# Performance work log

Hardware: AMD Instinct MI355X
Metric: run time of the kernel (lower is better)

Reference implementation:

```python
import jax, jax.numpy as jnp
import numpy as np


def setup_inputs() -> dict:
    key = jax.random.key(0)
    ks = jax.random.split(key, 9)
    B, Lq, Lk, D = 8, 2048, 2048, 768
    s = 1.0 / np.sqrt(D)
    return {
        "queries": jax.random.normal(ks[0], (B, Lq, D), dtype=jnp.float32),
        "values": jax.random.normal(ks[1], (B, Lk, D), dtype=jnp.float32),
        "mask": jax.random.randint(ks[2], (B, Lq, Lk), 0, 2) > 0,
        "Wq": jax.random.normal(ks[3], (D, D), dtype=jnp.float32) * s,
        "bq": jax.random.normal(ks[4], (D,), dtype=jnp.float32) * s,
        "Wk": jax.random.normal(ks[5], (D, D), dtype=jnp.float32) * s,
        "bk": jax.random.normal(ks[6], (D,), dtype=jnp.float32) * s,
        "Wv": jax.random.normal(ks[7], (D, D), dtype=jnp.float32) * s,
        "bv": jax.random.normal(ks[8], (D,), dtype=jnp.float32) * s,
    }


def reference(queries, values, mask, Wq, bq, Wk, bk, Wv, bv):
    NEG = jnp.asarray(-1e9, queries.dtype)
    # torch Linear: x @ W.T + b
    q = jnp.einsum("bld,ed->ble", queries, Wq) + bq
    v = jnp.einsum("bld,ed->ble", values, Wv) + bv
    # NOTE (faithful to source): keys are the key-projection of the
    # already value-projected tensor.
    k = jnp.einsum("bld,ed->ble", v, Wk) + bk
    score = jnp.einsum("bqd,bkd->bqk", q, k)  # [B, Lq, Lk]
    score = jnp.where(mask, score, NEG)
    attn = jax.nn.sigmoid(score)  # sigmoid attention, no normalization
    context = jnp.einsum("bqk,bkd->bqd", attn, v)
    return context
```

## Files before the change

### kernel.cpp

```cpp
#include <hip/hip_runtime.h>
#include <hip/hip_bf16.h>

typedef __bf16 bf16_t;
typedef __bf16 bf16x8 __attribute__((ext_vector_type(8)));
typedef __bf16 bf16x4 __attribute__((ext_vector_type(4)));
typedef float  f32x4  __attribute__((ext_vector_type(4)));

#define LDS_DST(p) ((__attribute__((address_space(3))) void*)(p))
#define GLB_SRC(p) ((const __attribute__((address_space(1))) void*)(p))

#define SBAR()   asm volatile("s_barrier" ::: "memory")
#define WVM8()   asm volatile("s_waitcnt vmcnt(8)" ::: "memory")
#define WVM4()   asm volatile("s_waitcnt vmcnt(4)" ::: "memory")
#define WVM0()   asm volatile("s_waitcnt vmcnt(0)" ::: "memory")
#define SP1()    __builtin_amdgcn_s_setprio(1)
#define SP0()    __builtin_amdgcn_s_setprio(0)

__global__ void __launch_bounds__(256)
convert_kernel(const float* __restrict__ q_in, const float* __restrict__ v_in,
               const float* __restrict__ wq_in, const float* __restrict__ wk_in,
               const float* __restrict__ wv_in,
               bf16_t* __restrict__ qb, bf16_t* __restrict__ vb,
               bf16_t* __restrict__ wqb, bf16_t* __restrict__ wkb,
               bf16_t* __restrict__ wvb) {
  const int tid = threadIdx.x;
  int r = blockIdx.x;
  const float* in; bf16_t* out; int base;
  if (r < 6144) {
    in = (r < 3072) ? q_in : v_in;
    out = (r < 3072) ? qb : vb;
    base = (r % 3072) * 1024;
  } else {
    r -= 6144;
    in = (r < 144) ? wq_in : (r < 288 ? wk_in : wv_in);
    out = (r < 144) ? wqb : (r < 288 ? wkb : wvb);
    base = (r % 144) * 1024;
  }
#pragma unroll
  for (int j = 0; j < 4; ++j) {
    const int i = base + j * 256 + tid;
    const float4 v = reinterpret_cast<const float4*>(in)[i];
    bf16x4 o;
    o[0] = (bf16_t)v.x; o[1] = (bf16_t)v.y; o[2] = (bf16_t)v.z; o[3] = (bf16_t)v.w;
    reinterpret_cast<bf16x4*>(out)[i] = o;
  }
}

__global__ void __launch_bounds__(256)
transpose_bf16_kernel(const bf16_t* __restrict__ in, bf16_t* __restrict__ out,
                      int R, int C) {
  __shared__ bf16_t tile[64][72];
  const long base = (long)blockIdx.z * R * C;
  const bf16_t* ib = in + base;
  bf16_t* ob = out + base;
  const int r0 = blockIdx.x * 64, c0 = blockIdx.y * 64;
  const int tid = threadIdx.x;
  const int rr = tid >> 3, cg = tid & 7;
#pragma unroll
  for (int p = 0; p < 2; ++p) {
    int row = p * 32 + rr;
    bf16x8 v = *reinterpret_cast<const bf16x8*>(ib + (long)(r0 + row) * C + c0 + cg * 8);
    *reinterpret_cast<bf16x8*>(&tile[row][cg * 8]) = v;
  }
  __syncthreads();
#pragma unroll
  for (int p = 0; p < 2; ++p) {
    int c = p * 32 + rr;
    bf16x8 v;
#pragma unroll
    for (int i = 0; i < 8; ++i) v[i] = tile[cg * 8 + i][c];
    *reinterpret_cast<bf16x8*>(ob + (long)(c0 + c) * R + r0 + cg * 8) = v;
  }
}


__device__ __forceinline__ void read_A(const char* smem, int off, bf16x8 (&af)[8], int xk0) {
#pragma unroll
  for (int mf = 0; mf < 4; ++mf)
#pragma unroll
    for (int kk = 0; kk < 2; ++kk)
      af[mf * 2 + kk] = *reinterpret_cast<const bf16x8*>(
          smem + off + mf * 2048 + (kk ? (xk0 ^ 64) : xk0));
}

__device__ __forceinline__ void read_B(const char* smem, int off, bf16x8 (&bf_)[4], int xk0) {
#pragma unroll
  for (int nf = 0; nf < 2; ++nf)
#pragma unroll
    for (int kk = 0; kk < 2; ++kk)
      bf_[nf * 2 + kk] = *reinterpret_cast<const bf16x8*>(
          smem + off + nf * 2048 + (kk ? (xk0 ^ 64) : xk0));
}

template <int MH, int NH>
__device__ __forceinline__ void mfma_q(const bf16x8 (&af)[8], const bf16x8 (&bf_)[4],
                                       f32x4 (&acc)[8][4]) {
#pragma unroll
  for (int mf = 0; mf < 4; ++mf)
#pragma unroll
    for (int nf = 0; nf < 2; ++nf)
#pragma unroll
      for (int kk = 0; kk < 2; ++kk)
        acc[MH * 4 + mf][NH * 2 + nf] = __builtin_amdgcn_mfma_f32_16x16x32_bf16(
            af[mf * 2 + kk], bf_[nf * 2 + kk], acc[MH * 4 + mf][NH * 2 + nf], 0, 0, 0);
}

#define STAGE_A(slot, mh, kt) do {                                            \
  _Pragma("unroll") for (int j_ = 0; j_ < 2; ++j_)                            \
    __builtin_amdgcn_global_load_lds(                                         \
        GLB_SRC(pA + (long)(j_ * 128 + (mh) * 64) * K + (kt)),                \
        LDS_DST(smem + (slot) * 65536 + (arow0 + j_ * 128 + (mh) * 64) * 128),\
        16, 0, 0);                                                            \
} while (0)

#define STAGE_B(slot, nh, kt) do {                                            \
  _Pragma("unroll") for (int j_ = 0; j_ < 2; ++j_)                            \
    __builtin_amdgcn_global_load_lds(                                         \
        GLB_SRC(pB + (long)(j_ * 128 + (nh) * 32) * K + (kt)),                \
        LDS_DST(smem + (slot) * 65536 + 32768 +                               \
                (brow0 + j_ * 128 + (nh) * 32) * 128),                        \
        16, 0, 0);                                                            \
} while (0)

#define EWRITE(RD, eb) do {                                                   \
  _Pragma("unroll") for (int fi = 0; fi < 2; ++fi)                            \
  _Pragma("unroll") for (int nf = 0; nf < 4; ++nf)                            \
  _Pragma("unroll") for (int r = 0; r < 4; ++r) {                             \
    const int lr2 = wr * 32 + fi * 16 + lg * 4 + r;                           \
    (eb)[lr2 * 256 + wc * 64 + nf * 16 + l15] = acc[(RD) * 2 + fi][nf][r];    \
  }                                                                           \
} while (0)

template <int MODE>
__global__ void __launch_bounds__(512, 2)
gemm8p_kernel(const bf16_t* __restrict__ A, const bf16_t* __restrict__ B,
              const float* __restrict__ bias, const int* __restrict__ mask,
              void* __restrict__ Cout, int M, int N, int K,
              long sA, long sB, long sC, long sMask,
              const bf16_t* __restrict__ A2, const bf16_t* __restrict__ B2,
              const float* __restrict__ bias2, void* __restrict__ C2) {
  __shared__ __align__(1024) char smem[131072];

  const int gx = gridDim.x, gy = gridDim.y;
  int f0 = blockIdx.x + gx * (blockIdx.y + gy * blockIdx.z);
  const int nwg = gx * gy * (int)gridDim.z;
  const int q8 = nwg >> 3, r8 = nwg & 7;
  const int xcd = f0 & 7, idx = f0 >> 3;
  int f1 = (xcd < r8 ? xcd * (q8 + 1) : r8 * (q8 + 1) + (xcd - r8) * q8) + idx;
  int bxi, byi, bz;
  if constexpr (MODE == 1) {
    bxi = f1 & 7;
    const int byL = (f1 >> 3) & 1;
    const int st = (f1 >> 4) & 3;
    bz = f1 >> 6;
    byi = st * 2 + byL;
  } else {
    byi = f1 % gy;
    const int t = f1 / gy;
    bxi = t % gx;
    bz = t / gx;
  }

  const bf16_t* Ab; const bf16_t* Bb;
  const float* biasp = bias; void* Cp = Cout;
  if constexpr (MODE == 0) {
    if (bz) { Ab = A2; Bb = B2; biasp = bias2; Cp = C2; }
    else    { Ab = A;  Bb = B; }
  } else {
    Ab = A + bz * sA; Bb = B + bz * sB;
  }
  const int bm = bxi * 256, bn = byi * 256;
  const int tid = threadIdx.x;
  const int wave = tid >> 6, lane = tid & 63;
  const int wr = wave >> 2, wc = wave & 3;
  const int l15 = lane & 15, lg = lane >> 4;
  const int xk0 = (lg * 16) ^ ((lane & 7) << 4);
  const int NT = K >> 6;

  const int lr = lane >> 3;
  const int cgs = ((lane & 7) ^ lr) * 8;
  const int arow0 = wave * 8;
  const int brow0 = (wave >> 2) * 64 + (wave & 3) * 8;
  const bf16_t* pA = Ab + (long)(bm + arow0 + lr) * K + cgs;
  const bf16_t* pB = Bb + (long)(bn + brow0 + lr) * K + cgs;

  const int aoff = wr * 16384 + l15 * 128;
  const int boff = 32768 + wc * 8192 + l15 * 128;

  f32x4 acc[8][4] = {};
  bf16x8 afX[8], bfB[4], bf0[4];

  STAGE_A(0, 0, 0); STAGE_B(0, 0, 0); STAGE_B(0, 1, 0); STAGE_A(0, 1, 0);
  STAGE_A(1, 0, 64); STAGE_B(1, 0, 64);
  STAGE_B(1, 1, 64); STAGE_A(1, 1, 64);
  WVM8();
  SBAR();
  read_A(smem, aoff + 0, afX, xk0);
  read_B(smem, boff + 0, bf0, xk0);

  int slot = 0;
  for (int t = 0; t + 2 < NT; ++t) {
    const int so = slot * 65536, sn = (slot ^ 1) * 65536;
    const int k2 = (t + 2) << 6;
    read_B(smem, so + boff + 4096, bfB, xk0);
    STAGE_A(slot, 0, k2); STAGE_B(slot, 0, k2);
    SP1(); mfma_q<0, 0>(afX, bf0, acc); SP0();
    SP1(); mfma_q<0, 1>(afX, bfB, acc); SP0();
    read_A(smem, so + aoff + 8192, afX, xk0);
    WVM8(); SBAR();
    SP1(); mfma_q<1, 1>(afX, bfB, acc); SP0();
    SP1(); mfma_q<1, 0>(afX, bf0, acc); SP0();
    read_A(smem, sn + aoff + 0, afX, xk0);
    read_B(smem, sn + boff + 0, bf0, xk0);
    STAGE_B(slot, 1, k2); STAGE_A(slot, 1, k2);
    WVM8(); SBAR();
    slot ^= 1;
  }

  {
    const int so = slot * 65536, sn = (slot ^ 1) * 65536;
    read_B(smem, so + boff + 4096, bfB, xk0);
    SP1(); mfma_q<0, 0>(afX, bf0, acc); SP0();
    SP1(); mfma_q<0, 1>(afX, bfB, acc); SP0();
    read_A(smem, so + aoff + 8192, afX, xk0);
    WVM4(); SBAR();
    SP1(); mfma_q<1, 1>(afX, bfB, acc); SP0();
    SP1(); mfma_q<1, 0>(afX, bf0, acc); SP0();
    read_A(smem, sn + aoff + 0, afX, xk0);
    read_B(smem, sn + boff + 0, bf0, xk0);
    WVM0(); SBAR();
    read_B(smem, sn + boff + 4096, bfB, xk0);
    SP1(); mfma_q<0, 0>(afX, bf0, acc); SP0();
    SP1(); mfma_q<0, 1>(afX, bfB, acc); SP0();
    read_A(smem, sn + aoff + 8192, afX, xk0);
    SP1(); mfma_q<1, 1>(afX, bfB, acc); SP0();
    SP1(); mfma_q<1, 0>(afX, bf0, acc); SP0();
  }

  float* eb0 = (float*)smem;
  float* eb1 = (float*)(smem + 65536);
  const int lrow = tid >> 3, t7 = tid & 7;
  const int growt0 = lrow + ((lrow >> 5) * 96);
  int4 m4a[8], m4b[8];
  if constexpr (MODE == 1) {
    const int* mrow = mask + bz * sMask + (long)(bm + growt0) * N + bn;
#pragma unroll
    for (int q = 0; q < 8; ++q)
      m4a[q] = *reinterpret_cast<const int4*>(mrow + (q * 8 + t7) * 4);
  }
  EWRITE(0, eb0);
  __syncthreads();
#pragma unroll
  for (int rd = 0; rd < 4; ++rd) {
    if constexpr (MODE == 1) {
      if (rd < 3) {
        const int* mrow =
            mask + bz * sMask + (long)(bm + (rd + 1) * 32 + growt0) * N + bn;
        if ((rd & 1) == 0) {
#pragma unroll
          for (int q = 0; q < 8; ++q)
            m4b[q] = *reinterpret_cast<const int4*>(mrow + (q * 8 + t7) * 4);
        } else {
#pragma unroll
          for (int q = 0; q < 8; ++q)
            m4a[q] = *reinterpret_cast<const int4*>(mrow + (q * 8 + t7) * 4);
        }
      }
    }
    if (rd < 3) {
      if ((rd & 1) == 0) { EWRITE(rd + 1, eb1); } else { EWRITE(rd + 1, eb0); }
    }
    const float* eb = ((rd & 1) == 0) ? eb0 : eb1;
    const long rowbase = (long)(bm + rd * 32 + growt0) * N + bn;
#pragma unroll
    for (int q = 0; q < 8; ++q) {
      const int c4 = (q * 8 + t7) * 4;
      const f32x4 v = *reinterpret_cast<const f32x4*>(&eb[lrow * 256 + c4]);
      if constexpr (MODE == 1) {
        const int4 mq = ((rd & 1) == 0) ? m4a[q] : m4b[q];
        bf16x4 o;
        o[0] = (bf16_t)(mq.x ? __builtin_amdgcn_rcpf(1.f + __expf(-v[0])) : 0.f);
        o[1] = (bf16_t)(mq.y ? __builtin_amdgcn_rcpf(1.f + __expf(-v[1])) : 0.f);
        o[2] = (bf16_t)(mq.z ? __builtin_amdgcn_rcpf(1.f + __expf(-v[2])) : 0.f);
        o[3] = (bf16_t)(mq.w ? __builtin_amdgcn_rcpf(1.f + __expf(-v[3])) : 0.f);
        *reinterpret_cast<bf16x4*>((bf16_t*)Cp + bz * sC + rowbase + c4) = o;
      } else if constexpr (MODE == 0) {
        const f32x4 b4 = *reinterpret_cast<const f32x4*>(biasp + bn + c4);
        bf16x4 o;
        o[0] = (bf16_t)(v[0] + b4[0]); o[1] = (bf16_t)(v[1] + b4[1]);
        o[2] = (bf16_t)(v[2] + b4[2]); o[3] = (bf16_t)(v[3] + b4[3]);
        *reinterpret_cast<bf16x4*>((bf16_t*)Cp + bz * sC + rowbase + c4) = o;
      } else {
        *reinterpret_cast<f32x4*>((float*)Cp + bz * sC + rowbase + c4) = v;
      }
    }
    __syncthreads();
  }
}

extern "C" void kernel_launch(void* const* d_in, const int* in_sizes, int n_in,
                              void* d_out, int out_size, void* d_ws, size_t ws_size,
                              hipStream_t stream) {
  const float* queries = (const float*)d_in[0];
  const float* values  = (const float*)d_in[1];
  const int*   mask    = (const int*)d_in[2];
  const float* Wq = (const float*)d_in[3];
  const float* bq = (const float*)d_in[4];
  const float* Wk = (const float*)d_in[5];
  const float* bk = (const float*)d_in[6];
  const float* Wv = (const float*)d_in[7];
  const float* bv = (const float*)d_in[8];

  char* ws = (char*)d_ws;
  bf16_t* qb  = (bf16_t*)(ws + 0);
  bf16_t* vb  = (bf16_t*)(ws + 25165824);
  bf16_t* wqb = (bf16_t*)(ws + 50331648);
  bf16_t* wkb = (bf16_t*)(ws + 51511296);
  bf16_t* wvb = (bf16_t*)(ws + 52690944);
  bf16_t* qp  = (bf16_t*)(ws + 53870592);
  bf16_t* vp  = (bf16_t*)(ws + 79036416);
  bf16_t* kp  = (bf16_t*)(ws + 104202240);
  bf16_t* vpT = (bf16_t*)(ws + 129368064);
  bf16_t* P   = (bf16_t*)(ws + 154533888);

  convert_kernel<<<6576, 256, 0, stream>>>(queries, values, Wq, Wk, Wv,
                                           qb, vb, wqb, wkb, wvb);

  const dim3 blk2(512);

  gemm8p_kernel<0><<<dim3(64, 3, 2), blk2, 0, stream>>>(
      qb, wqb, bq, nullptr, qp, 16384, 768, 768, 0, 0, 0, 0,
      vb, wvb, bv, vp);
  gemm8p_kernel<0><<<dim3(64, 3, 1), blk2, 0, stream>>>(
      vp, wkb, bk, nullptr, kp, 16384, 768, 768, 0, 0, 0, 0,
      vp, wkb, bk, kp);

  transpose_bf16_kernel<<<dim3(32, 12, 8), 256, 0, stream>>>(vp, vpT, 2048, 768);

  gemm8p_kernel<1><<<dim3(8, 8, 8), blk2, 0, stream>>>(
      qp, kp, nullptr, mask, P, 2048, 2048, 768,
      (long)2048 * 768, (long)2048 * 768, (long)2048 * 2048, (long)2048 * 2048,
      nullptr, nullptr, nullptr, nullptr);

  gemm8p_kernel<2><<<dim3(8, 3, 8), blk2, 0, stream>>>(
      P, vpT, nullptr, nullptr, d_out, 2048, 768, 2048,
      (long)2048 * 2048, (long)768 * 2048, (long)2048 * 768, 0,
      nullptr, nullptr, nullptr, nullptr);
}
```

Baseline: 253.5 us.

## Fuse V transpose into the V-projection GEMM epilogue and swizzle epilogue LDS

Removes the standalone bf16 transpose kernel. The V-projection GEMM epilogue now also writes a transposed copy of its output (with bias) straight to vpT, reading it back from the staged LDS tile. The MODE 0 epilogue staging buffer gains an XOR swizzle so that the column-wise reads avoid bank conflicts. This saves one launch and a full read and write of vp, but adds strided 16-byte global stores and extra LDS reads to the projection epilogue.

```diff
diff --git a/kernel.cpp b/kernel.cpp
--- a/kernel.cpp
+++ b/kernel.cpp
@@ -46,33 +46,6 @@
   }
 }
 
-__global__ void __launch_bounds__(256)
-transpose_bf16_kernel(const bf16_t* __restrict__ in, bf16_t* __restrict__ out,
-                      int R, int C) {
-  __shared__ bf16_t tile[64][72];
-  const long base = (long)blockIdx.z * R * C;
-  const bf16_t* ib = in + base;
-  bf16_t* ob = out + base;
-  const int r0 = blockIdx.x * 64, c0 = blockIdx.y * 64;
-  const int tid = threadIdx.x;
-  const int rr = tid >> 3, cg = tid & 7;
-#pragma unroll
-  for (int p = 0; p < 2; ++p) {
-    int row = p * 32 + rr;
-    bf16x8 v = *reinterpret_cast<const bf16x8*>(ib + (long)(r0 + row) * C + c0 + cg * 8);
-    *reinterpret_cast<bf16x8*>(&tile[row][cg * 8]) = v;
-  }
-  __syncthreads();
-#pragma unroll
-  for (int p = 0; p < 2; ++p) {
-    int c = p * 32 + rr;
-    bf16x8 v;
-#pragma unroll
-    for (int i = 0; i < 8; ++i) v[i] = tile[cg * 8 + i][c];
-    *reinterpret_cast<bf16x8*>(ob + (long)(c0 + c) * R + r0 + cg * 8) = v;
-  }
-}
-
 
 __device__ __forceinline__ void read_A(const char* smem, int off, bf16x8 (&af)[8], int xk0) {
 #pragma unroll
@@ -131,6 +104,16 @@
   }                                                                           \
 } while (0)
 
+#define EWRITE_S(RD, eb) do {                                                 \
+  _Pragma("unroll") for (int fi = 0; fi < 2; ++fi)                            \
+  _Pragma("unroll") for (int nf = 0; nf < 4; ++nf)                            \
+  _Pragma("unroll") for (int r = 0; r < 4; ++r) {                             \
+    const int lr2 = wr * 32 + fi * 16 + lg * 4 + r;                           \
+    const int cS = (wc * 64 + nf * 16 + l15) ^ ((lr2 & 7) << 2);              \
+    (eb)[lr2 * 256 + cS] = acc[(RD) * 2 + fi][nf][r];                         \
+  }                                                                           \
+} while (0)
+
 template <int MODE>
 __global__ void __launch_bounds__(512, 2)
 gemm8p_kernel(const bf16_t* __restrict__ A, const bf16_t* __restrict__ B,
@@ -138,7 +121,8 @@
               void* __restrict__ Cout, int M, int N, int K,
               long sA, long sB, long sC, long sMask,
               const bf16_t* __restrict__ A2, const bf16_t* __restrict__ B2,
-              const float* __restrict__ bias2, void* __restrict__ C2) {
+              const float* __restrict__ bias2, void* __restrict__ C2,
+              bf16_t* __restrict__ Ct) {
   __shared__ __align__(1024) char smem[131072];
 
   const int gx = gridDim.x, gy = gridDim.y;
@@ -241,6 +225,7 @@
   float* eb1 = (float*)(smem + 65536);
   const int lrow = tid >> 3, t7 = tid & 7;
   const int growt0 = lrow + ((lrow >> 5) * 96);
+  const bool doT = (MODE == 0) && (bz != 0) && (Ct != nullptr);
   int4 m4a[8], m4b[8];
   if constexpr (MODE == 1) {
     const int* mrow = mask + bz * sMask + (long)(bm + growt0) * N + bn;
@@ -248,7 +233,7 @@
     for (int q = 0; q < 8; ++q)
       m4a[q] = *reinterpret_cast<const int4*>(mrow + (q * 8 + t7) * 4);
   }
-  EWRITE(0, eb0);
+  if constexpr (MODE == 0) { EWRITE_S(0, eb0); } else { EWRITE(0, eb0); }
   __syncthreads();
 #pragma unroll
   for (int rd = 0; rd < 4; ++rd) {
@@ -268,14 +253,19 @@
       }
     }
     if (rd < 3) {
-      if ((rd & 1) == 0) { EWRITE(rd + 1, eb1); } else { EWRITE(rd + 1, eb0); }
+      if constexpr (MODE == 0) {
+        if ((rd & 1) == 0) { EWRITE_S(rd + 1, eb1); } else { EWRITE_S(rd + 1, eb0); }
+      } else {
+        if ((rd & 1) == 0) { EWRITE(rd + 1, eb1); } else { EWRITE(rd + 1, eb0); }
+      }
     }
     const float* eb = ((rd & 1) == 0) ? eb0 : eb1;
     const long rowbase = (long)(bm + rd * 32 + growt0) * N + bn;
 #pragma unroll
     for (int q = 0; q < 8; ++q) {
       const int c4 = (q * 8 + t7) * 4;
-      const f32x4 v = *reinterpret_cast<const f32x4*>(&eb[lrow * 256 + c4]);
+      const int cR = (MODE == 0) ? (c4 ^ ((lrow & 7) << 2)) : c4;
+      const f32x4 v = *reinterpret_cast<const f32x4*>(&eb[lrow * 256 + cR]);
       if constexpr (MODE == 1) {
         const int4 mq = ((rd & 1) == 0) ? m4a[q] : m4b[q];
         bf16x4 o;
@@ -294,6 +284,23 @@
         *reinterpret_cast<f32x4*>((float*)Cp + bz * sC + rowbase + c4) = v;
       }
     }
+    if constexpr (MODE == 0) {
+      if (doT) {
+        const int colT = tid & 255, g = tid >> 8;
+        const float bT = biasp[bn + colT];
+        bf16_t tv[32];
+#pragma unroll
+        for (int r = 0; r < 32; ++r)
+          tv[r] = (bf16_t)(eb[(g * 32 + r) * 256 + (colT ^ ((r & 7) << 2))] + bT);
+        bf16_t* dst = Ct + (long)(bm >> 11) * (768L * 2048)
+                      + (long)(bn + colT) * 2048
+                      + (bm & 2047) + g * 128 + rd * 32;
+#pragma unroll
+        for (int j = 0; j < 4; ++j)
+          *reinterpret_cast<bf16x8*>(dst + j * 8) =
+              *reinterpret_cast<const bf16x8*>(&tv[j * 8]);
+      }
+    }
     __syncthreads();
   }
 }
@@ -330,20 +337,18 @@
 
   gemm8p_kernel<0><<<dim3(64, 3, 2), blk2, 0, stream>>>(
       qb, wqb, bq, nullptr, qp, 16384, 768, 768, 0, 0, 0, 0,
-      vb, wvb, bv, vp);
+      vb, wvb, bv, vp, vpT);
   gemm8p_kernel<0><<<dim3(64, 3, 1), blk2, 0, stream>>>(
       vp, wkb, bk, nullptr, kp, 16384, 768, 768, 0, 0, 0, 0,
-      vp, wkb, bk, kp);
-
-  transpose_bf16_kernel<<<dim3(32, 12, 8), 256, 0, stream>>>(vp, vpT, 2048, 768);
+      vp, wkb, bk, kp, nullptr);
 
   gemm8p_kernel<1><<<dim3(8, 8, 8), blk2, 0, stream>>>(
       qp, kp, nullptr, mask, P, 2048, 2048, 768,
       (long)2048 * 768, (long)2048 * 768, (long)2048 * 2048, (long)2048 * 2048,
-      nullptr, nullptr, nullptr, nullptr);
+      nullptr, nullptr, nullptr, nullptr, nullptr);
 
   gemm8p_kernel<2><<<dim3(8, 3, 8), blk2, 0, stream>>>(
       P, vpT, nullptr, nullptr, d_out, 2048, 768, 2048,
       (long)2048 * 2048, (long)768 * 2048, (long)2048 * 768, 0,
-      nullptr, nullptr, nullptr, nullptr);
-}
+      nullptr, nullptr, nullptr, nullptr, nullptr);
+}
```

Result: slower. 261.7 us (+3.2%).

## Merge V transpose into K-projection GEMM launch via extra workgroups

Applied to the files above, without the earlier changes.

Adds a MODE 3 GEMM variant whose grid holds 256 workgroups: the first 192 compute the K projection (vp·Wk + bk), and the remaining 64 each transpose 48 64x64 tiles of vp into vpT through LDS. This removes a separate transpose kernel launch and lets the transpose run alongside the GEMM, filling CUs the 192-tile GEMM leaves idle. The trade-off is that the transpose blocks reserve the GEMM's large 128 KB LDS allocation and 512-thread blocks, and each block loops serially with two barriers per tile.

```diff
diff --git a/kernel.cpp b/kernel.cpp
--- a/kernel.cpp
+++ b/kernel.cpp
@@ -46,33 +46,6 @@
   }
 }
 
-__global__ void __launch_bounds__(256)
-transpose_bf16_kernel(const bf16_t* __restrict__ in, bf16_t* __restrict__ out,
-                      int R, int C) {
-  __shared__ bf16_t tile[64][72];
-  const long base = (long)blockIdx.z * R * C;
-  const bf16_t* ib = in + base;
-  bf16_t* ob = out + base;
-  const int r0 = blockIdx.x * 64, c0 = blockIdx.y * 64;
-  const int tid = threadIdx.x;
-  const int rr = tid >> 3, cg = tid & 7;
-#pragma unroll
-  for (int p = 0; p < 2; ++p) {
-    int row = p * 32 + rr;
-    bf16x8 v = *reinterpret_cast<const bf16x8*>(ib + (long)(r0 + row) * C + c0 + cg * 8);
-    *reinterpret_cast<bf16x8*>(&tile[row][cg * 8]) = v;
-  }
-  __syncthreads();
-#pragma unroll
-  for (int p = 0; p < 2; ++p) {
-    int c = p * 32 + rr;
-    bf16x8 v;
-#pragma unroll
-    for (int i = 0; i < 8; ++i) v[i] = tile[cg * 8 + i][c];
-    *reinterpret_cast<bf16x8*>(ob + (long)(c0 + c) * R + r0 + cg * 8) = v;
-  }
-}
-
 
 __device__ __forceinline__ void read_A(const char* smem, int off, bf16x8 (&af)[8], int xk0) {
 #pragma unroll
@@ -140,6 +113,7 @@
               const bf16_t* __restrict__ A2, const bf16_t* __restrict__ B2,
               const float* __restrict__ bias2, void* __restrict__ C2) {
   __shared__ __align__(1024) char smem[131072];
+  constexpr int EM = (MODE == 3) ? 0 : MODE;
 
   const int gx = gridDim.x, gy = gridDim.y;
   int f0 = blockIdx.x + gx * (blockIdx.y + gy * blockIdx.z);
@@ -148,7 +122,36 @@
   const int xcd = f0 & 7, idx = f0 >> 3;
   int f1 = (xcd < r8 ? xcd * (q8 + 1) : r8 * (q8 + 1) + (xcd - r8) * q8) + idx;
   int bxi, byi, bz;
-  if constexpr (MODE == 1) {
+  if constexpr (MODE == 3) {
+    if (f1 >= 192) {
+      bf16_t (*tile)[72] = (bf16_t(*)[72])smem;
+      bf16_t* vpT = (bf16_t*)C2;
+      const int tid_ = threadIdx.x;
+      const int rr = tid_ >> 3, cg = tid_ & 7;
+      const int tt = f1 - 192;
+      for (int i = 0; i < 48; ++i) {
+        const int tau = tt * 48 + i;
+        const int z = tau / 384, rem = tau % 384;
+        const int rx = rem % 32, cy = rem / 32;
+        const long base = (long)z * 2048 * 768;
+        const bf16_t* ib = A + base;
+        bf16_t* ob = vpT + base;
+        const int r0 = rx * 64, c0 = cy * 64;
+        __syncthreads();
+        *reinterpret_cast<bf16x8*>(&tile[rr][cg * 8]) =
+            *reinterpret_cast<const bf16x8*>(ib + (long)(r0 + rr) * 768 + c0 + cg * 8);
+        __syncthreads();
+        bf16x8 v;
+#pragma unroll
+        for (int e = 0; e < 8; ++e) v[e] = tile[cg * 8 + e][rr];
+        *reinterpret_cast<bf16x8*>(ob + (long)(c0 + rr) * 2048 + r0 + cg * 8) = v;
+      }
+      return;
+    }
+    byi = f1 % 3;
+    bxi = f1 / 3;
+    bz = 0;
+  } else if constexpr (MODE == 1) {
     bxi = f1 & 7;
     const int byL = (f1 >> 3) & 1;
     const int st = (f1 >> 4) & 3;
@@ -163,9 +166,9 @@
 
   const bf16_t* Ab; const bf16_t* Bb;
   const float* biasp = bias; void* Cp = Cout;
-  if constexpr (MODE == 0) {
-    if (bz) { Ab = A2; Bb = B2; biasp = bias2; Cp = C2; }
-    else    { Ab = A;  Bb = B; }
+  if constexpr (EM == 0) {
+    if (MODE == 0 && bz) { Ab = A2; Bb = B2; biasp = bias2; Cp = C2; }
+    else                 { Ab = A;  Bb = B; }
   } else {
     Ab = A + bz * sA; Bb = B + bz * sB;
   }
@@ -242,7 +245,7 @@
   const int lrow = tid >> 3, t7 = tid & 7;
   const int growt0 = lrow + ((lrow >> 5) * 96);
   int4 m4a[8], m4b[8];
-  if constexpr (MODE == 1) {
+  if constexpr (EM == 1) {
     const int* mrow = mask + bz * sMask + (long)(bm + growt0) * N + bn;
 #pragma unroll
     for (int q = 0; q < 8; ++q)
@@ -252,7 +255,7 @@
   __syncthreads();
 #pragma unroll
   for (int rd = 0; rd < 4; ++rd) {
-    if constexpr (MODE == 1) {
+    if constexpr (EM == 1) {
       if (rd < 3) {
         const int* mrow =
             mask + bz * sMask + (long)(bm + (rd + 1) * 32 + growt0) * N + bn;
@@ -276,7 +279,7 @@
     for (int q = 0; q < 8; ++q) {
       const int c4 = (q * 8 + t7) * 4;
       const f32x4 v = *reinterpret_cast<const f32x4*>(&eb[lrow * 256 + c4]);
-      if constexpr (MODE == 1) {
+      if constexpr (EM == 1) {
         const int4 mq = ((rd & 1) == 0) ? m4a[q] : m4b[q];
         bf16x4 o;
         o[0] = (bf16_t)(mq.x ? __builtin_amdgcn_rcpf(1.f + __expf(-v[0])) : 0.f);
@@ -284,7 +287,7 @@
         o[2] = (bf16_t)(mq.z ? __builtin_amdgcn_rcpf(1.f + __expf(-v[2])) : 0.f);
         o[3] = (bf16_t)(mq.w ? __builtin_amdgcn_rcpf(1.f + __expf(-v[3])) : 0.f);
         *reinterpret_cast<bf16x4*>((bf16_t*)Cp + bz * sC + rowbase + c4) = o;
-      } else if constexpr (MODE == 0) {
+      } else if constexpr (EM == 0) {
         const f32x4 b4 = *reinterpret_cast<const f32x4*>(biasp + bn + c4);
         bf16x4 o;
         o[0] = (bf16_t)(v[0] + b4[0]); o[1] = (bf16_t)(v[1] + b4[1]);
@@ -331,11 +334,9 @@
   gemm8p_kernel<0><<<dim3(64, 3, 2), blk2, 0, stream>>>(
       qb, wqb, bq, nullptr, qp, 16384, 768, 768, 0, 0, 0, 0,
       vb, wvb, bv, vp);
-  gemm8p_kernel<0><<<dim3(64, 3, 1), blk2, 0, stream>>>(
+  gemm8p_kernel<3><<<dim3(256, 1, 1), blk2, 0, stream>>>(
       vp, wkb, bk, nullptr, kp, 16384, 768, 768, 0, 0, 0, 0,
-      vp, wkb, bk, kp);
-
-  transpose_bf16_kernel<<<dim3(32, 12, 8), 256, 0, stream>>>(vp, vpT, 2048, 768);
+      nullptr, nullptr, nullptr, vpT);
 
   gemm8p_kernel<1><<<dim3(8, 8, 8), blk2, 0, stream>>>(
       qp, kp, nullptr, mask, P, 2048, 2048, 768,
```

New measurement: 264.4 us. 1.04x slower.
